# Optimization experiments

Measured on AMD Instinct MI355X. Metric: run time of the kernel, lower is better.

Reference implementation:

```python
import jax, jax.numpy as jnp
import numpy as np

MAX_NORM = 1.0
B, V, C, VOCAB, E = 256, 50, 32, 100000, 128


def setup_inputs() -> dict:
    key = jax.random.key(0)
    k1, k2, k3 = jax.random.split(key, 3)
    W = jax.random.normal(k1, (VOCAB, E), dtype=jnp.float32)
    codes = jax.random.randint(k2, (B, V, C), 0, VOCAB, dtype=jnp.int64)
    n_visits = jax.random.randint(k3, (B,), 1, V + 1, dtype=jnp.int64)
    # ensure batch_max_visits == V (static output shape, matches min(max(len), max_visits))
    n_visits = n_visits.at[0].set(V)
    return {"W": W, "codes": codes, "n_visits": n_visits}


def reference(W, codes, n_visits):
    # Faithful to the torch module: expand_visits produces offsets [0,1,...,nv-1],
    # so EmbeddingBag('sum') bag i = emb(flat[i]) for i < nv-1, and the last bag
    # sums emb(flat[nv-1 : nv*C]). Result is top-padded to V rows per patient.
    b, v, c = codes.shape
    L = v * c
    flat = codes.reshape(b, L)                     # flattened codes per patient
    g = W[flat]                                    # [B, L, E] gathered rows
    # EmbeddingBag max_norm: renormalize looked-up rows whose norm exceeds MAX_NORM
    norms = jnp.linalg.norm(g, axis=-1, keepdims=True)
    g = g * jnp.minimum(1.0, MAX_NORM / jnp.maximum(norms, 1e-12))
    # prefix sums: cs0[:, j] = sum of g[:, :j]
    cs0 = jnp.concatenate([jnp.zeros((b, 1, g.shape[-1]), g.dtype),
                           jnp.cumsum(g, axis=1)], axis=1)  # [B, L+1, E]
    nv = n_visits.astype(jnp.int32)                # [B]
    end = (nv * c)[:, None, None]                  # sum over real flattened codes
    start = (nv - 1)[:, None, None]
    S = (jnp.take_along_axis(cs0, end, axis=1)
         - jnp.take_along_axis(cs0, start, axis=1))  # [B, 1, E] last-bag sum
    r = jnp.arange(v, dtype=jnp.int32)[None, :]    # output row index
    i = r - (v - nv[:, None])                      # bag index (negative => pad row)
    ei = jnp.take_along_axis(g, jnp.clip(i, 0, L - 1)[:, :, None], axis=1)  # [B, V, E]
    out = jnp.where((i >= 0)[:, :, None],
                    jnp.where((i < nv[:, None] - 1)[:, :, None], ei, S),
                    jnp.zeros_like(ei))
    return out
```

## Files before the change

### kernel.cpp

```cpp
#include <hip/hip_runtime.h>
#include <math.h>

#define B_     256
#define V_     50
#define C_     32
#define E_     128
#define VOCAB_ 100000
#define L_     (V_ * C_)
#define SPB    8
#define NCHUNK (SPB * 4)

__global__ __launch_bounds__(256, 6) void fused_kernel(
    const float* __restrict__ W,
    const int*   __restrict__ codes,
    const int*   __restrict__ nvis,
    float*       __restrict__ out)
{
    const int tid  = threadIdx.x;
    const int wave = tid >> 6;
    const int lane = tid & 63;
    const int g    = lane >> 4;
    const int l4   = lane & 15;

    const int b  = blockIdx.x >> 3;
    const int s  = blockIdx.x & (SPB - 1);
    const int nv = nvis[b];
    const int* cf = codes + b * L_;
    float* ob = out + (size_t)b * V_ * E_;

    {
        const int i = (wave * 4 + g) * SPB + s;
        if (i < V_ - 1) {
            if (i < nv - 1) {
                const int code = cf[i];
                const float* row = W + (size_t)code * E_;
                float4 v1 = ((const float4*)row)[l4];
                float4 v2 = ((const float4*)row)[16 + l4];
                float ss = v1.x*v1.x + v1.y*v1.y + v1.z*v1.z + v1.w*v1.w
                         + v2.x*v2.x + v2.y*v2.y + v2.z*v2.z + v2.w*v2.w;
                #pragma unroll
                for (int m = 1; m <= 8; m <<= 1) ss += __shfl_xor(ss, m, 64);
                const float sc = fminf(1.0f, 1.0f / fmaxf(sqrtf(ss), 1e-12f));
                float* orow = ob + (size_t)(V_ - nv + i) * E_;
                ((float4*)orow)[l4]      = make_float4(v1.x*sc, v1.y*sc, v1.z*sc, v1.w*sc);
                ((float4*)orow)[16 + l4] = make_float4(v2.x*sc, v2.y*sc, v2.z*sc, v2.w*sc);
            } else {
                float* orow = ob + (size_t)(i - (nv - 1)) * E_;
                ((float4*)orow)[l4]      = make_float4(0.f, 0.f, 0.f, 0.f);
                ((float4*)orow)[16 + l4] = make_float4(0.f, 0.f, 0.f, 0.f);
            }
        }
    }

    const int j0    = nv - 1;
    const int j1    = nv * C_;
    const int chunk = (j1 - j0 + NCHUNK - 1) / NCHUNK;
    const int wid   = s * 4 + wave;
    const int a0    = j0 + wid * chunk;
    const int n     = min(a0 + chunk, j1) - a0;

    int cl = 0;
    if (lane < n) cl = cf[a0 + lane];

    float4 a1 = make_float4(0.f, 0.f, 0.f, 0.f);
    float4 a2 = make_float4(0.f, 0.f, 0.f, 0.f);
    #pragma unroll 4
    for (int t = 0; t < n; t += 4) {
        const int tt   = t + g;
        const int code = __shfl(cl, tt, 64);
        const float* row = W + (size_t)code * E_;
        float4 v1 = ((const float4*)row)[l4];
        float4 v2 = ((const float4*)row)[16 + l4];
        float ss = v1.x*v1.x + v1.y*v1.y + v1.z*v1.z + v1.w*v1.w
                 + v2.x*v2.x + v2.y*v2.y + v2.z*v2.z + v2.w*v2.w;
        #pragma unroll
        for (int m = 1; m <= 8; m <<= 1) ss += __shfl_xor(ss, m, 64);
        float sc = fminf(1.0f, 1.0f / fmaxf(sqrtf(ss), 1e-12f));
        if (tt >= n) sc = 0.0f;
        a1.x += v1.x*sc; a1.y += v1.y*sc; a1.z += v1.z*sc; a1.w += v1.w*sc;
        a2.x += v2.x*sc; a2.y += v2.y*sc; a2.z += v2.z*sc; a2.w += v2.w*sc;
    }

    #pragma unroll
    for (int m = 16; m <= 32; m <<= 1) {
        a1.x += __shfl_xor(a1.x, m, 64); a1.y += __shfl_xor(a1.y, m, 64);
        a1.z += __shfl_xor(a1.z, m, 64); a1.w += __shfl_xor(a1.w, m, 64);
        a2.x += __shfl_xor(a2.x, m, 64); a2.y += __shfl_xor(a2.y, m, 64);
        a2.z += __shfl_xor(a2.z, m, 64); a2.w += __shfl_xor(a2.w, m, 64);
    }

    __shared__ float4 s1[4][16], s2[4][16];
    if (lane < 16) { s1[wave][l4] = a1; s2[wave][l4] = a2; }
    __syncthreads();
    if (tid < 16) {
        float4 f1 = s1[0][l4], f2 = s2[0][l4];
        #pragma unroll
        for (int w = 1; w < 4; w++) {
            f1.x += s1[w][l4].x; f1.y += s1[w][l4].y;
            f1.z += s1[w][l4].z; f1.w += s1[w][l4].w;
            f2.x += s2[w][l4].x; f2.y += s2[w][l4].y;
            f2.z += s2[w][l4].z; f2.w += s2[w][l4].w;
        }
        float* dst = ob + (size_t)(V_ - 1) * E_;
        atomicAdd(&dst[4*l4 + 0], f1.x);
        atomicAdd(&dst[4*l4 + 1], f1.y);
        atomicAdd(&dst[4*l4 + 2], f1.z);
        atomicAdd(&dst[4*l4 + 3], f1.w);
        atomicAdd(&dst[64 + 4*l4 + 0], f2.x);
        atomicAdd(&dst[64 + 4*l4 + 1], f2.y);
        atomicAdd(&dst[64 + 4*l4 + 2], f2.z);
        atomicAdd(&dst[64 + 4*l4 + 3], f2.w);
    }
}

extern "C" void kernel_launch(void* const* d_in, const int* in_sizes, int n_in,
                              void* d_out, int out_size, void* d_ws, size_t ws_size,
                              hipStream_t stream) {
    const float* W     = (const float*)d_in[0];
    const int*   codes = (const int*)d_in[1];
    const int*   nvis  = (const int*)d_in[2];
    float*       out   = (float*)d_out;

    fused_kernel<<<B_ * SPB, 256, 0, stream>>>(W, codes, nvis, out);
}
```

Measured before the change: 98.26 us.

## Pre-normalize the embedding table into bf16, then gather the half-width rows

A new first kernel reads the whole fp32 embedding table, applies the max_norm rescale per row, and writes a bf16 copy into workspace. The gather kernel then reads 256-byte bf16 rows and widens them to fp32 with bit shifts. This removes the per-gather norm reduction and halves the bytes fetched per looked-up row. In exchange it adds a full pass over the table on every call, and it loses precision: the last bag sums hundreds of rounded rows, which may exceed tolerance.

```diff
diff --git a/kernel.cpp b/kernel.cpp
--- a/kernel.cpp
+++ b/kernel.cpp
@@ -10,11 +10,37 @@
 #define SPB    8
 #define NCHUNK (SPB * 4)
 
-__global__ __launch_bounds__(256, 6) void fused_kernel(
-    const float* __restrict__ W,
-    const int*   __restrict__ codes,
-    const int*   __restrict__ nvis,
-    float*       __restrict__ out)
+
+__device__ __forceinline__ unsigned short f2bf(float f) {
+    unsigned u = __float_as_uint(f);
+    unsigned r = (u + 0x7fffu + ((u >> 16) & 1u)) >> 16;
+    return (unsigned short)r;
+}
+
+__global__ __launch_bounds__(256) void convert_kernel(
+    const float* __restrict__ W, unsigned short* __restrict__ T)
+{
+    const int hw = blockIdx.x * 8 + (threadIdx.x >> 5);
+    const int hl = threadIdx.x & 31;
+    const float* row = W + (size_t)hw * E_;
+    float4 v = ((const float4*)row)[hl];
+    float ss = v.x * v.x + v.y * v.y + v.z * v.z + v.w * v.w;
+    #pragma unroll
+    for (int m = 1; m <= 16; m <<= 1) ss += __shfl_xor(ss, m, 64);
+    const float sc = fminf(1.0f, 1.0f / fmaxf(sqrtf(ss), 1e-12f));
+    ushort4 p;
+    p.x = f2bf(v.x * sc);
+    p.y = f2bf(v.y * sc);
+    p.z = f2bf(v.z * sc);
+    p.w = f2bf(v.w * sc);
+    ((ushort4*)(T + (size_t)hw * E_))[hl] = p;
+}
+
+__global__ __launch_bounds__(256, 6) void gather_kernel(
+    const unsigned short* __restrict__ T,
+    const int* __restrict__ codes,
+    const int* __restrict__ nvis,
+    float* __restrict__ out)
 {
     const int tid  = threadIdx.x;
     const int wave = tid >> 6;
@@ -33,21 +59,18 @@
         if (i < V_ - 1) {
             if (i < nv - 1) {
                 const int code = cf[i];
-                const float* row = W + (size_t)code * E_;
-                float4 v1 = ((const float4*)row)[l4];
-                float4 v2 = ((const float4*)row)[16 + l4];
-                float ss = v1.x*v1.x + v1.y*v1.y + v1.z*v1.z + v1.w*v1.w
-                         + v2.x*v2.x + v2.y*v2.y + v2.z*v2.z + v2.w*v2.w;
-                #pragma unroll
-                for (int m = 1; m <= 8; m <<= 1) ss += __shfl_xor(ss, m, 64);
-                const float sc = fminf(1.0f, 1.0f / fmaxf(sqrtf(ss), 1e-12f));
+                uint4 u = ((const uint4*)(T + (size_t)code * E_))[l4];
                 float* orow = ob + (size_t)(V_ - nv + i) * E_;
-                ((float4*)orow)[l4]      = make_float4(v1.x*sc, v1.y*sc, v1.z*sc, v1.w*sc);
-                ((float4*)orow)[16 + l4] = make_float4(v2.x*sc, v2.y*sc, v2.z*sc, v2.w*sc);
+                ((float4*)orow)[2 * l4] = make_float4(
+                    __uint_as_float(u.x << 16), __uint_as_float(u.x & 0xffff0000u),
+                    __uint_as_float(u.y << 16), __uint_as_float(u.y & 0xffff0000u));
+                ((float4*)orow)[2 * l4 + 1] = make_float4(
+                    __uint_as_float(u.z << 16), __uint_as_float(u.z & 0xffff0000u),
+                    __uint_as_float(u.w << 16), __uint_as_float(u.w & 0xffff0000u));
             } else {
                 float* orow = ob + (size_t)(i - (nv - 1)) * E_;
-                ((float4*)orow)[l4]      = make_float4(0.f, 0.f, 0.f, 0.f);
-                ((float4*)orow)[16 + l4] = make_float4(0.f, 0.f, 0.f, 0.f);
+                ((float4*)orow)[2 * l4]     = make_float4(0.f, 0.f, 0.f, 0.f);
+                ((float4*)orow)[2 * l4 + 1] = make_float4(0.f, 0.f, 0.f, 0.f);
             }
         }
     }
@@ -62,54 +85,56 @@
     int cl = 0;
     if (lane < n) cl = cf[a0 + lane];
 
-    float4 a1 = make_float4(0.f, 0.f, 0.f, 0.f);
-    float4 a2 = make_float4(0.f, 0.f, 0.f, 0.f);
+    float a00 = 0.f, a1 = 0.f, a2 = 0.f, a3 = 0.f;
+    float a4 = 0.f, a5 = 0.f, a6 = 0.f, a7 = 0.f;
     #pragma unroll 4
     for (int t = 0; t < n; t += 4) {
         const int tt   = t + g;
         const int code = __shfl(cl, tt, 64);
-        const float* row = W + (size_t)code * E_;
-        float4 v1 = ((const float4*)row)[l4];
-        float4 v2 = ((const float4*)row)[16 + l4];
-        float ss = v1.x*v1.x + v1.y*v1.y + v1.z*v1.z + v1.w*v1.w
-                 + v2.x*v2.x + v2.y*v2.y + v2.z*v2.z + v2.w*v2.w;
-        #pragma unroll
-        for (int m = 1; m <= 8; m <<= 1) ss += __shfl_xor(ss, m, 64);
-        float sc = fminf(1.0f, 1.0f / fmaxf(sqrtf(ss), 1e-12f));
-        if (tt >= n) sc = 0.0f;
-        a1.x += v1.x*sc; a1.y += v1.y*sc; a1.z += v1.z*sc; a1.w += v1.w*sc;
-        a2.x += v2.x*sc; a2.y += v2.y*sc; a2.z += v2.z*sc; a2.w += v2.w*sc;
+        uint4 u = ((const uint4*)(T + (size_t)code * E_))[l4];
+        const float valid = (tt < n) ? 1.0f : 0.0f;
+        a00 += __uint_as_float(u.x << 16)          * valid;
+        a1  += __uint_as_float(u.x & 0xffff0000u)  * valid;
+        a2  += __uint_as_float(u.y << 16)          * valid;
+        a3  += __uint_as_float(u.y & 0xffff0000u)  * valid;
+        a4  += __uint_as_float(u.z << 16)          * valid;
+        a5  += __uint_as_float(u.z & 0xffff0000u)  * valid;
+        a6  += __uint_as_float(u.w << 16)          * valid;
+        a7  += __uint_as_float(u.w & 0xffff0000u)  * valid;
     }
 
     #pragma unroll
     for (int m = 16; m <= 32; m <<= 1) {
-        a1.x += __shfl_xor(a1.x, m, 64); a1.y += __shfl_xor(a1.y, m, 64);
-        a1.z += __shfl_xor(a1.z, m, 64); a1.w += __shfl_xor(a1.w, m, 64);
-        a2.x += __shfl_xor(a2.x, m, 64); a2.y += __shfl_xor(a2.y, m, 64);
-        a2.z += __shfl_xor(a2.z, m, 64); a2.w += __shfl_xor(a2.w, m, 64);
+        a00 += __shfl_xor(a00, m, 64); a1 += __shfl_xor(a1, m, 64);
+        a2  += __shfl_xor(a2, m, 64);  a3 += __shfl_xor(a3, m, 64);
+        a4  += __shfl_xor(a4, m, 64);  a5 += __shfl_xor(a5, m, 64);
+        a6  += __shfl_xor(a6, m, 64);  a7 += __shfl_xor(a7, m, 64);
     }
 
-    __shared__ float4 s1[4][16], s2[4][16];
-    if (lane < 16) { s1[wave][l4] = a1; s2[wave][l4] = a2; }
+    __shared__ float4 sA[4][16], sB[4][16];
+    if (lane < 16) {
+        sA[wave][l4] = make_float4(a00, a1, a2, a3);
+        sB[wave][l4] = make_float4(a4, a5, a6, a7);
+    }
     __syncthreads();
     if (tid < 16) {
-        float4 f1 = s1[0][l4], f2 = s2[0][l4];
+        float4 f1 = sA[0][l4], f2 = sB[0][l4];
         #pragma unroll
         for (int w = 1; w < 4; w++) {
-            f1.x += s1[w][l4].x; f1.y += s1[w][l4].y;
-            f1.z += s1[w][l4].z; f1.w += s1[w][l4].w;
-            f2.x += s2[w][l4].x; f2.y += s2[w][l4].y;
-            f2.z += s2[w][l4].z; f2.w += s2[w][l4].w;
+            f1.x += sA[w][l4].x; f1.y += sA[w][l4].y;
+            f1.z += sA[w][l4].z; f1.w += sA[w][l4].w;
+            f2.x += sB[w][l4].x; f2.y += sB[w][l4].y;
+            f2.z += sB[w][l4].z; f2.w += sB[w][l4].w;
         }
-        float* dst = ob + (size_t)(V_ - 1) * E_;
-        atomicAdd(&dst[4*l4 + 0], f1.x);
-        atomicAdd(&dst[4*l4 + 1], f1.y);
-        atomicAdd(&dst[4*l4 + 2], f1.z);
-        atomicAdd(&dst[4*l4 + 3], f1.w);
-        atomicAdd(&dst[64 + 4*l4 + 0], f2.x);
-        atomicAdd(&dst[64 + 4*l4 + 1], f2.y);
-        atomicAdd(&dst[64 + 4*l4 + 2], f2.z);
-        atomicAdd(&dst[64 + 4*l4 + 3], f2.w);
+        float* dst = ob + (size_t)(V_ - 1) * E_ + 8 * l4;
+        atomicAdd(&dst[0], f1.x);
+        atomicAdd(&dst[1], f1.y);
+        atomicAdd(&dst[2], f1.z);
+        atomicAdd(&dst[3], f1.w);
+        atomicAdd(&dst[4], f2.x);
+        atomicAdd(&dst[5], f2.y);
+        atomicAdd(&dst[6], f2.z);
+        atomicAdd(&dst[7], f2.w);
     }
 }
 
@@ -120,6 +145,8 @@
     const int*   codes = (const int*)d_in[1];
     const int*   nvis  = (const int*)d_in[2];
     float*       out   = (float*)d_out;
+    unsigned short* T  = (unsigned short*)d_ws;
 
-    fused_kernel<<<B_ * SPB, 256, 0, stream>>>(W, codes, nvis, out);
+    convert_kernel<<<VOCAB_ / 8, 256, 0, stream>>>(W, T);
+    gather_kernel<<<B_ * SPB, 256, 0, stream>>>(T, codes, nvis, out);
 }
```

After: 113.2 us. 1.15x slower.
